# Kernel optimization log

Measured on AMD Instinct MI355X. Metric: run time of the kernel, lower is better.

## Reference

```python
import jax, jax.numpy as jnp
import numpy as np
from jax import lax

BN_EPS = 1e-5


def setup_inputs() -> dict:
    key = jax.random.key(0)
    ks = jax.random.split(key, 8)
    B, C, H, W = 2, 256, 64, 64
    Cr = C // 4
    return {
        "x": jax.random.normal(ks[0], (B, C, H, W), jnp.float32),
        "conv_w": jax.random.normal(ks[1], (Cr, C, 3, 3), jnp.float32) * 0.02,
        "conv_b": jax.random.normal(ks[2], (Cr,), jnp.float32) * 0.02,
        "bn_gamma": jax.random.uniform(ks[3], (Cr,), jnp.float32, 0.5, 1.5),
        "bn_beta": jax.random.normal(ks[4], (Cr,), jnp.float32) * 0.1,
        "bn_mean": jax.random.normal(ks[5], (Cr,), jnp.float32) * 0.1,
        "bn_var": jax.random.uniform(ks[6], (Cr,), jnp.float32, 0.5, 1.5),
        "prelu_w": jnp.full((1,), 0.25, jnp.float32),
    }


def reference(x, conv_w, conv_b, bn_gamma, bn_beta, bn_mean, bn_var, prelu_w):
    B, C, H, W = x.shape
    N = H * W
    # conv_match: 3x3 conv (pad=1) -> BatchNorm (inference) -> PReLU
    y = lax.conv_general_dilated(
        x, conv_w, window_strides=(1, 1), padding="SAME",
        dimension_numbers=("NCHW", "OIHW", "NCHW"))
    y = y + conv_b[None, :, None, None]
    scale = bn_gamma / jnp.sqrt(bn_var + BN_EPS)
    y = (y - bn_mean[None, :, None, None]) * scale[None, :, None, None] + bn_beta[None, :, None, None]
    y = jnp.where(y >= 0, y, prelu_w[0] * y)  # PReLU, single shared slope

    e = y.reshape(B, -1, N)                       # [B, Cr, N]
    sim = jnp.einsum("bdn,bdm->bnm", e, e)        # [B, N, N]
    sim = sim - jnp.max(sim, axis=2, keepdims=True)

    # sparsemax along last dim
    srt = -jnp.sort(-sim, axis=2)                 # descending sort
    cs = jnp.cumsum(srt, axis=2) - 1.0
    ar = jnp.arange(1, N + 1, dtype=sim.dtype)[None, None, :]
    mask = ar * srt > cs
    k = jnp.sum(mask, axis=2, keepdims=True)      # int support size, [B,N,1]
    tau = jnp.take_along_axis(cs, k - 1, axis=2) / k.astype(sim.dtype)
    p = jnp.maximum(sim - tau, 0.0)               # sparsemax probs [B,N,N]

    out = jnp.einsum("bcn,bnm->bcm", x.reshape(B, C, N), p)
    return out.reshape(B, C, H, W) + x
```

## Files before the change

### kernel.cpp

```cpp
#include <hip/hip_runtime.h>
#include <math.h>

#define NPIX 4096
#define CR   64
#define CIN  256
#define HW   64
#define CSPLIT 8

typedef __attribute__((ext_vector_type(8))) short s16x8;
typedef __attribute__((ext_vector_type(4))) float f32x4;

__device__ __forceinline__ unsigned short f2bf(float f) {
  union { float f; unsigned u; } a; a.f = f;
  return (unsigned short)((a.u + 0x7FFF + ((a.u >> 16) & 1)) >> 16);
}
__device__ __forceinline__ float bf2f(unsigned short h) {
  union { unsigned u; float f; } a; a.u = (unsigned)h << 16; return a.f;
}

__global__ __launch_bounds__(256) void k_conv_part(
    const float* __restrict__ x, const float* __restrict__ cw,
    float* __restrict__ pp) {
  const int hg = blockIdx.x;
  const int dg = blockIdx.y;
  const int b  = blockIdx.z >> 3;
  const int cs = blockIdx.z & 7;
  const int h0 = hg * 2, d0 = dg * 32, c0 = cs * 32;
  const int tid = threadIdx.x;
  const int wp = tid & 31;
  const int dq = tid >> 5;
  const int w0 = wp * 2;

  __shared__ float xs[16][4][68];
  __shared__ float wl[16][9][32];

  float acc[2][2][4] = {};

  for (int cc = 0; cc < 32; cc += 16) {
    __syncthreads();
    for (int i = tid; i < 16 * 256; i += 256) {
      int c = i >> 8, r = (i >> 6) & 3, w = i & 63;
      int row = h0 - 1 + r;
      float v = 0.f;
      if (row >= 0 && row < HW)
        v = x[((size_t)(b * CIN + c0 + cc + c) << 12) + row * HW + w];
      xs[c][r][w + 1] = v;
    }
    if (tid < 128) {
      int c = tid >> 3, r = (tid >> 1) & 3, s = tid & 1;
      xs[c][r][s ? 65 : 0] = 0.f;
    }
    for (int i = tid; i < 16 * 9 * 32; i += 256) {
      int c = i / 288, rem = i - c * 288, tap = rem >> 5, d = rem & 31;
      wl[c][tap][d] = cw[(size_t)(d0 + d) * 2304 + (c0 + cc + c) * 9 + tap];
    }
    __syncthreads();

#pragma unroll 2
    for (int c = 0; c < 16; ++c) {
      float xv[4][4];
#pragma unroll
      for (int r = 0; r < 4; ++r) {
        float2 p0 = *(const float2*)&xs[c][r][w0];
        float2 p1 = *(const float2*)&xs[c][r][w0 + 2];
        xv[r][0] = p0.x; xv[r][1] = p0.y; xv[r][2] = p1.x; xv[r][3] = p1.y;
      }
#pragma unroll
      for (int tap = 0; tap < 9; ++tap) {
        const int kh = tap / 3, kw = tap - kh * 3;
        float4 wv = *(const float4*)&wl[c][tap][dq * 4];
        float wf[4] = {wv.x, wv.y, wv.z, wv.w};
#pragma unroll
        for (int hi = 0; hi < 2; ++hi)
#pragma unroll
          for (int wi = 0; wi < 2; ++wi) {
            float xvv = xv[hi + kh][wi + kw];
#pragma unroll
            for (int di = 0; di < 4; ++di)
              acc[hi][wi][di] = fmaf(wf[di], xvv, acc[hi][wi][di]);
          }
      }
    }
  }
#pragma unroll
  for (int di = 0; di < 4; ++di) {
    int d = d0 + dq * 4 + di;
#pragma unroll
    for (int hi = 0; hi < 2; ++hi)
#pragma unroll
      for (int wi = 0; wi < 2; ++wi)
        pp[((size_t)((b * CSPLIT + cs) * 64 + d) << 12) + (h0 + hi) * HW + w0 + wi] =
            acc[hi][wi][di];
  }
}

__global__ __launch_bounds__(256) void k_bn(
    const float* __restrict__ pp, const float* __restrict__ cb,
    const float* __restrict__ gamma, const float* __restrict__ beta,
    const float* __restrict__ mean, const float* __restrict__ var,
    const float* __restrict__ pw, unsigned short* __restrict__ eTh,
    unsigned short* __restrict__ eTl) {
  const int n0 = blockIdx.x * 64;
  const int b  = blockIdx.y;
  const int tid = threadIdx.x;
  __shared__ float et[64][65];

  const float slope = pw[0];
#pragma unroll 4
  for (int dd = 0; dd < 16; ++dd) {
    int d = dd * 4 + (tid >> 6);
    int n = tid & 63;
    float s = 0.f;
#pragma unroll
    for (int cs = 0; cs < CSPLIT; ++cs)
      s += pp[((size_t)((b * CSPLIT + cs) * 64 + d) << 12) + n0 + n];
    float scale = gamma[d] / sqrtf(var[d] + 1e-5f);
    float y = (s + cb[d] - mean[d]) * scale + beta[d];
    y = (y >= 0.f) ? y : slope * y;
    et[d][n] = y;
  }
  __syncthreads();
#pragma unroll 4
  for (int w = 0; w < 16; ++w) {
    int n = w * 4 + (tid >> 6);
    int d = tid & 63;
    float v = et[d][n];
    unsigned short hi = f2bf(v);
    unsigned short lo = f2bf(v - bf2f(hi));
    int nl = n0 + n;
    int g = nl >> 8, i = nl & 255;
    int np = (g << 8) | ((i & 15) << 4) | (i >> 4);
    size_t off = (((size_t)b << 12) + np) * 64 + d;
    eTh[off] = hi;
    eTl[off] = lo;
  }
}

__global__ __launch_bounds__(1024) void k_gsm(
    const unsigned short* __restrict__ eTh, const unsigned short* __restrict__ eTl,
    unsigned short* __restrict__ p, unsigned char* __restrict__ flags) {
  const int n0 = blockIdx.x * 16;
  const int b  = blockIdx.y;
  const int tid = threadIdx.x;
  const int l = tid & 63, wid = tid >> 6;
  const int lc = l & 15, lq = l >> 4;

  __shared__ __align__(16) unsigned short eah[16][72];
  __shared__ __align__(16) unsigned short eal[16][72];
  __shared__ float rs[16][16];
  __shared__ int   rc[16][16];
  __shared__ float stau[16];
  __shared__ int   sprev[16];
  __shared__ int   schg;

  const size_t ebase = ((size_t)b << 12) * 64;

  {
    int d = tid & 63, r = (tid >> 6) & 15;
    int g = n0 >> 8, a = (n0 & 255) >> 4;
    int np = (g << 8) | (r << 4) | a;
    size_t off = ebase + (size_t)np * 64 + d;
    eah[r][d] = eTh[off];
    eal[r][d] = eTl[off];
  }
  if (tid < 16) sprev[tid] = NPIX + 1;
  __syncthreads();

  f32x4 acc[16];
#pragma unroll
  for (int t = 0; t < 16; ++t)
#pragma unroll
    for (int q = 0; q < 4; ++q) acc[t][q] = 0.f;

  const int mbase = wid * 256;
#pragma unroll
  for (int kc = 0; kc < 2; ++kc) {
    s16x8 ah = *(const s16x8*)&eah[lc][kc * 32 + lq * 8];
    s16x8 al = *(const s16x8*)&eal[lc][kc * 32 + lq * 8];
#pragma unroll
    for (int t = 0; t < 16; ++t) {
      size_t off = ebase + (size_t)(mbase + t * 16 + lc) * 64 + kc * 32 + lq * 8;
      s16x8 bh = *(const s16x8*)&eTh[off];
      s16x8 bl = *(const s16x8*)&eTl[off];
      acc[t] = __builtin_amdgcn_mfma_f32_16x16x32_bf16(ah, bh, acc[t], 0, 0, 0);
      acc[t] = __builtin_amdgcn_mfma_f32_16x16x32_bf16(ah, bl, acc[t], 0, 0, 0);
      acc[t] = __builtin_amdgcn_mfma_f32_16x16x32_bf16(al, bh, acc[t], 0, 0, 0);
    }
  }

  {
    float mx[4];
#pragma unroll
    for (int q = 0; q < 4; ++q) {
      float m = acc[0][q];
#pragma unroll
      for (int t = 1; t < 16; ++t) m = fmaxf(m, acc[t][q]);
      mx[q] = m;
    }
#pragma unroll
    for (int o = 1; o <= 8; o <<= 1)
#pragma unroll
      for (int q = 0; q < 4; ++q) mx[q] = fmaxf(mx[q], __shfl_xor(mx[q], o));
    if (lc == 0)
#pragma unroll
      for (int q = 0; q < 4; ++q) rs[wid][lq * 4 + q] = mx[q];
  }
  __syncthreads();
  if (tid < 16) {
    float m = rs[0][tid];
#pragma unroll
    for (int w = 1; w < 16; ++w) m = fmaxf(m, rs[w][tid]);
    stau[tid] = m - 1.0f;
  }

  for (int it = 0; it < 64; ++it) {
    __syncthreads();
    float tl[4];
#pragma unroll
    for (int q = 0; q < 4; ++q) tl[q] = stau[lq * 4 + q];
    if (tid == 0) schg = 0;
    float s[4]; int c[4];
#pragma unroll
    for (int q = 0; q < 4; ++q) { s[q] = 0.f; c[q] = 0; }
#pragma unroll
    for (int t = 0; t < 16; ++t)
#pragma unroll
      for (int q = 0; q < 4; ++q) {
        float v = acc[t][q];
        if (v > tl[q]) { s[q] += v; ++c[q]; }
      }
#pragma unroll
    for (int o = 1; o <= 8; o <<= 1)
#pragma unroll
      for (int q = 0; q < 4; ++q) {
        s[q] += __shfl_xor(s[q], o);
        c[q] += __shfl_xor(c[q], o);
      }
    if (lc == 0)
#pragma unroll
      for (int q = 0; q < 4; ++q) { rs[wid][lq * 4 + q] = s[q]; rc[wid][lq * 4 + q] = c[q]; }
    __syncthreads();
    if (tid < 16) {
      float ss = 0.f; int cc = 0;
#pragma unroll
      for (int w = 0; w < 16; ++w) { ss += rs[w][tid]; cc += rc[w][tid]; }
      stau[tid] = (ss - 1.f) / (float)cc;
      if (cc != sprev[tid]) { sprev[tid] = cc; schg = 1; }
    }
    __syncthreads();
    if (schg == 0) break;
  }

  float tw[4];
#pragma unroll
  for (int q = 0; q < 4; ++q) tw[q] = stau[lq * 4 + q];
  s16x8 oA[4], oB[4];
  int anyL = 0;
#pragma unroll
  for (int q = 0; q < 4; ++q) {
#pragma unroll
    for (int t = 0; t < 8; ++t) {
      float pv = fmaxf(acc[t][q] - tw[q], 0.f);
      anyL |= (pv > 0.f);
      oA[q][t] = (short)f2bf(pv);
    }
#pragma unroll
    for (int t = 0; t < 8; ++t) {
      float pv = fmaxf(acc[t + 8][q] - tw[q], 0.f);
      anyL |= (pv > 0.f);
      oB[q][t] = (short)f2bf(pv);
    }
  }
  unsigned long long bal = __ballot(anyL != 0);
  const unsigned long long M0 = 0x00FF00FF00FF00FFULL;
  bool w0 = (bal & M0) != 0;
  bool w1 = (bal & ~M0) != 0;
  bool mine = (lc < 8) ? w0 : w1;
  if (mine) {
#pragma unroll
    for (int q = 0; q < 4; ++q) {
      unsigned short* pr =
          p + ((size_t)(b * NPIX + n0 + lq * 4 + q) << 12) + mbase + lc * 16;
      *(s16x8*)pr = oA[q];
      *(s16x8*)(pr + 8) = oB[q];
    }
  }
  if (l == 0) {
    int stripe = blockIdx.x;
    if (w0) flags[(b << 13) | ((wid * 2 + 0) << 8) | stripe] = 1;
    if (w1) flags[(b << 13) | ((wid * 2 + 1) << 8) | stripe] = 1;
  }
}

__global__ __launch_bounds__(256) void k_out_mfma(
    const unsigned short* __restrict__ pb, const float* __restrict__ x,
    float* __restrict__ out, const unsigned char* __restrict__ flags) {
  const int m0 = blockIdx.x * 128;
  const int c0 = blockIdx.y * 64;
  const int b  = blockIdx.z;
  const int tid = threadIdx.x;
  const int l = tid & 63, wid = tid >> 6;
  const int wr = wid >> 1, wc = wid & 1;

  __shared__ unsigned short As[64][42];
  __shared__ unsigned short Bs[128][42];
  __shared__ unsigned char fl[256];

  fl[tid] = flags[(b << 13) | (blockIdx.x << 8) | tid];

  f32x4 acc[2][4];
#pragma unroll
  for (int i = 0; i < 2; ++i)
#pragma unroll
    for (int j = 0; j < 4; ++j)
#pragma unroll
      for (int q = 0; q < 4; ++q) acc[i][j][q] = 0.f;

  const int arow = tid >> 2;
  const int akc  = (tid & 3) * 8;
  const float* axsrc = x + ((size_t)(b * CIN + c0 + arow) << 12) + akc;
  const int bm = (tid & 31) * 4;
  const int bk = (tid >> 5) * 4;
  const unsigned short* bsrc = pb + ((size_t)(b * NPIX + bk) << 12) + m0 + bm;
  const int myhalf = bk >> 4;

  __syncthreads();

  for (int k0 = 0; k0 < NPIX; k0 += 32) {
    const int s0 = k0 >> 4;
    const int have0 = fl[s0], have1 = fl[s0 + 1];
    if (!have0 && !have1) continue;
    __syncthreads();
    float4 A0 = *(const float4*)(axsrc + k0);
    float4 A1 = *(const float4*)(axsrc + k0 + 4);
    s16x8 ap;
    ap[0] = (short)f2bf(A0.x); ap[1] = (short)f2bf(A0.y);
    ap[2] = (short)f2bf(A0.z); ap[3] = (short)f2bf(A0.w);
    ap[4] = (short)f2bf(A1.x); ap[5] = (short)f2bf(A1.y);
    ap[6] = (short)f2bf(A1.z); ap[7] = (short)f2bf(A1.w);
    *(s16x8*)&As[arow][akc] = ap;
    if ((myhalf ? have1 : have0)) {
      const unsigned short* bp = bsrc + ((size_t)k0 << 12);
      ushort4 L0 = *(const ushort4*)(bp);
      ushort4 L1 = *(const ushort4*)(bp + 4096);
      ushort4 L2 = *(const ushort4*)(bp + 8192);
      ushort4 L3 = *(const ushort4*)(bp + 12288);
      *(ushort4*)&Bs[bm + 0][bk] = make_ushort4(L0.x, L1.x, L2.x, L3.x);
      *(ushort4*)&Bs[bm + 1][bk] = make_ushort4(L0.y, L1.y, L2.y, L3.y);
      *(ushort4*)&Bs[bm + 2][bk] = make_ushort4(L0.z, L1.z, L2.z, L3.z);
      *(ushort4*)&Bs[bm + 3][bk] = make_ushort4(L0.w, L1.w, L2.w, L3.w);
    } else {
      ushort4 zz = make_ushort4(0, 0, 0, 0);
      *(ushort4*)&Bs[bm + 0][bk] = zz;
      *(ushort4*)&Bs[bm + 1][bk] = zz;
      *(ushort4*)&Bs[bm + 2][bk] = zz;
      *(ushort4*)&Bs[bm + 3][bk] = zz;
    }
    __syncthreads();

    s16x8 a[2], bb[4];
    const int kg = l >> 4;
#pragma unroll
    for (int i = 0; i < 2; ++i) {
      int row = wr * 32 + i * 16 + (l & 15);
      a[i] = *(const s16x8*)&As[row][kg * 8];
    }
#pragma unroll
    for (int j = 0; j < 4; ++j) {
      int n = wc * 64 + j * 16 + (l & 15);
      bb[j] = *(const s16x8*)&Bs[n][kg * 8];
    }
#pragma unroll
    for (int i = 0; i < 2; ++i)
#pragma unroll
      for (int j = 0; j < 4; ++j)
        acc[i][j] = __builtin_amdgcn_mfma_f32_16x16x32_bf16(
            a[i], bb[j], acc[i][j], 0, 0, 0);
  }

#pragma unroll
  for (int i = 0; i < 2; ++i)
#pragma unroll
    for (int j = 0; j < 4; ++j)
#pragma unroll
      for (int q = 0; q < 4; ++q) {
        int c = c0 + wr * 32 + i * 16 + (l >> 4) * 4 + q;
        int m = m0 + wc * 64 + j * 16 + (l & 15);
        size_t off = ((size_t)(b * CIN + c) << 12) + m;
        out[off] = acc[i][j][q] + x[off];
      }
}

extern "C" void kernel_launch(void* const* d_in, const int* in_sizes, int n_in,
                              void* d_out, int out_size, void* d_ws, size_t ws_size,
                              hipStream_t stream) {
  const float* x     = (const float*)d_in[0];
  const float* cw    = (const float*)d_in[1];
  const float* cb    = (const float*)d_in[2];
  const float* gamma = (const float*)d_in[3];
  const float* beta  = (const float*)d_in[4];
  const float* mean  = (const float*)d_in[5];
  const float* var   = (const float*)d_in[6];
  const float* pw    = (const float*)d_in[7];
  float* out = (float*)d_out;

  unsigned short* p_bf = (unsigned short*)d_ws;
  float* pp  = (float*)((char*)d_ws + ((size_t)64 << 20));
  unsigned short* eTh = (unsigned short*)((char*)d_ws + ((size_t)80 << 20));
  unsigned short* eTl = (unsigned short*)((char*)d_ws + ((size_t)81 << 20));
  unsigned char* flags = (unsigned char*)((char*)d_ws + ((size_t)84 << 20));

  hipMemsetAsync(flags, 0, 2 * 32 * 256, stream);
  k_conv_part<<<dim3(32, 2, 16), 256, 0, stream>>>(x, cw, pp);
  k_bn<<<dim3(64, 2), 256, 0, stream>>>(pp, cb, gamma, beta, mean, var, pw,
                                        eTh, eTl);
  k_gsm<<<dim3(NPIX / 16, 2), 1024, 0, stream>>>(eTh, eTl, p_bf, flags);
  k_out_mfma<<<dim3(32, 4, 2), 256, 0, stream>>>(p_bf, x, out, flags);
}
```

Measured before the change: 287.1 us.

## Process 32 query rows per block in similarity-sparsemax kernel to reuse key loads

The fused similarity/sparsemax kernel now handles two 16-row groups per block instead of one. Each loaded key fragment (hi/lo bf16) feeds MFMAs for both groups, which halves global reads of the embedding matrix per output row and halves the grid size. The cost is double the accumulator registers (128 floats per lane) under a 1024-thread launch bound, which risks spills or lower occupancy. Fewer blocks also means less parallelism to hide latency.

After: 371.8 us. 1.29x slower.

```diff
diff --git a/kernel.cpp b/kernel.cpp
--- a/kernel.cpp
+++ b/kernel.cpp
@@ -139,74 +139,95 @@
 __global__ __launch_bounds__(1024) void k_gsm(
     const unsigned short* __restrict__ eTh, const unsigned short* __restrict__ eTl,
     unsigned short* __restrict__ p, unsigned char* __restrict__ flags) {
-  const int n0 = blockIdx.x * 16;
+  const int n0 = blockIdx.x * 32;
   const int b  = blockIdx.y;
   const int tid = threadIdx.x;
   const int l = tid & 63, wid = tid >> 6;
   const int lc = l & 15, lq = l >> 4;
 
-  __shared__ __align__(16) unsigned short eah[16][72];
-  __shared__ __align__(16) unsigned short eal[16][72];
-  __shared__ float rs[16][16];
-  __shared__ int   rc[16][16];
-  __shared__ float stau[16];
-  __shared__ int   sprev[16];
+  __shared__ __align__(16) unsigned short eah[32][72];
+  __shared__ __align__(16) unsigned short eal[32][72];
+  __shared__ float rs[16][32];
+  __shared__ int   rc[16][32];
+  __shared__ float stau[32];
+  __shared__ int   sprev[32];
   __shared__ int   schg;
 
   const size_t ebase = ((size_t)b << 12) * 64;
 
-  {
-    int d = tid & 63, r = (tid >> 6) & 15;
-    int g = n0 >> 8, a = (n0 & 255) >> 4;
-    int np = (g << 8) | (r << 4) | a;
+  for (int idx = tid; idx < 32 * 64; idx += 1024) {
+    int d = idx & 63, r = idx >> 6;
+    int nl = n0 + r;
+    int g = nl >> 8, i = nl & 255;
+    int np = (g << 8) | ((i & 15) << 4) | (i >> 4);
     size_t off = ebase + (size_t)np * 64 + d;
     eah[r][d] = eTh[off];
     eal[r][d] = eTl[off];
   }
-  if (tid < 16) sprev[tid] = NPIX + 1;
+  if (tid < 32) sprev[tid] = NPIX + 1;
   __syncthreads();
 
-  f32x4 acc[16];
-#pragma unroll
-  for (int t = 0; t < 16; ++t)
-#pragma unroll
-    for (int q = 0; q < 4; ++q) acc[t][q] = 0.f;
+  s16x8 Ah[2][2], Al[2][2];
+#pragma unroll
+  for (int g = 0; g < 2; ++g)
+#pragma unroll
+    for (int kc = 0; kc < 2; ++kc) {
+      Ah[g][kc] = *(const s16x8*)&eah[g * 16 + lc][kc * 32 + lq * 8];
+      Al[g][kc] = *(const s16x8*)&eal[g * 16 + lc][kc * 32 + lq * 8];
+    }
+
+  f32x4 acc[2][16];
+#pragma unroll
+  for (int g = 0; g < 2; ++g)
+#pragma unroll
+    for (int t = 0; t < 16; ++t)
+#pragma unroll
+      for (int q = 0; q < 4; ++q) acc[g][t][q] = 0.f;
 
   const int mbase = wid * 256;
-#pragma unroll
-  for (int kc = 0; kc < 2; ++kc) {
-    s16x8 ah = *(const s16x8*)&eah[lc][kc * 32 + lq * 8];
-    s16x8 al = *(const s16x8*)&eal[lc][kc * 32 + lq * 8];
-#pragma unroll
-    for (int t = 0; t < 16; ++t) {
-      size_t off = ebase + (size_t)(mbase + t * 16 + lc) * 64 + kc * 32 + lq * 8;
-      s16x8 bh = *(const s16x8*)&eTh[off];
-      s16x8 bl = *(const s16x8*)&eTl[off];
-      acc[t] = __builtin_amdgcn_mfma_f32_16x16x32_bf16(ah, bh, acc[t], 0, 0, 0);
-      acc[t] = __builtin_amdgcn_mfma_f32_16x16x32_bf16(ah, bl, acc[t], 0, 0, 0);
-      acc[t] = __builtin_amdgcn_mfma_f32_16x16x32_bf16(al, bh, acc[t], 0, 0, 0);
+#pragma unroll 4
+  for (int t = 0; t < 16; ++t) {
+    size_t off = ebase + (size_t)(mbase + t * 16 + lc) * 64 + lq * 8;
+    s16x8 bh0 = *(const s16x8*)&eTh[off];
+    s16x8 bh1 = *(const s16x8*)&eTh[off + 32];
+    s16x8 bl0 = *(const s16x8*)&eTl[off];
+    s16x8 bl1 = *(const s16x8*)&eTl[off + 32];
+#pragma unroll
+    for (int g = 0; g < 2; ++g) {
+      acc[g][t] = __builtin_amdgcn_mfma_f32_16x16x32_bf16(Ah[g][0], bh0, acc[g][t], 0, 0, 0);
+      acc[g][t] = __builtin_amdgcn_mfma_f32_16x16x32_bf16(Ah[g][0], bl0, acc[g][t], 0, 0, 0);
+      acc[g][t] = __builtin_amdgcn_mfma_f32_16x16x32_bf16(Al[g][0], bh0, acc[g][t], 0, 0, 0);
+      acc[g][t] = __builtin_amdgcn_mfma_f32_16x16x32_bf16(Ah[g][1], bh1, acc[g][t], 0, 0, 0);
+      acc[g][t] = __builtin_amdgcn_mfma_f32_16x16x32_bf16(Ah[g][1], bl1, acc[g][t], 0, 0, 0);
+      acc[g][t] = __builtin_amdgcn_mfma_f32_16x16x32_bf16(Al[g][1], bh1, acc[g][t], 0, 0, 0);
     }
   }
 
   {
-    float mx[4];
-#pragma unroll
-    for (int q = 0; q < 4; ++q) {
-      float m = acc[0][q];
-#pragma unroll
-      for (int t = 1; t < 16; ++t) m = fmaxf(m, acc[t][q]);
-      mx[q] = m;
-    }
+    float mx[2][4];
+#pragma unroll
+    for (int g = 0; g < 2; ++g)
+#pragma unroll
+      for (int q = 0; q < 4; ++q) {
+        float m = acc[g][0][q];
+#pragma unroll
+        for (int t = 1; t < 16; ++t) m = fmaxf(m, acc[g][t][q]);
+        mx[g][q] = m;
+      }
 #pragma unroll
     for (int o = 1; o <= 8; o <<= 1)
 #pragma unroll
-      for (int q = 0; q < 4; ++q) mx[q] = fmaxf(mx[q], __shfl_xor(mx[q], o));
+      for (int g = 0; g < 2; ++g)
+#pragma unroll
+        for (int q = 0; q < 4; ++q) mx[g][q] = fmaxf(mx[g][q], __shfl_xor(mx[g][q], o));
     if (lc == 0)
 #pragma unroll
-      for (int q = 0; q < 4; ++q) rs[wid][lq * 4 + q] = mx[q];
+      for (int g = 0; g < 2; ++g)
+#pragma unroll
+        for (int q = 0; q < 4; ++q) rs[wid][g * 16 + lq * 4 + q] = mx[g][q];
   }
   __syncthreads();
-  if (tid < 16) {
+  if (tid < 32) {
     float m = rs[0][tid];
 #pragma unroll
     for (int w = 1; w < 16; ++w) m = fmaxf(m, rs[w][tid]);
@@ -215,32 +236,45 @@
 
   for (int it = 0; it < 64; ++it) {
     __syncthreads();
-    float tl[4];
-#pragma unroll
-    for (int q = 0; q < 4; ++q) tl[q] = stau[lq * 4 + q];
+    float tl[2][4];
+#pragma unroll
+    for (int g = 0; g < 2; ++g)
+#pragma unroll
+      for (int q = 0; q < 4; ++q) tl[g][q] = stau[g * 16 + lq * 4 + q];
     if (tid == 0) schg = 0;
-    float s[4]; int c[4];
-#pragma unroll
-    for (int q = 0; q < 4; ++q) { s[q] = 0.f; c[q] = 0; }
+    float s[2][4]; int c[2][4];
+#pragma unroll
+    for (int g = 0; g < 2; ++g)
+#pragma unroll
+      for (int q = 0; q < 4; ++q) { s[g][q] = 0.f; c[g][q] = 0; }
 #pragma unroll
     for (int t = 0; t < 16; ++t)
 #pragma unroll
-      for (int q = 0; q < 4; ++q) {
-        float v = acc[t][q];
-        if (v > tl[q]) { s[q] += v; ++c[q]; }
-      }
+      for (int g = 0; g < 2; ++g)
+#pragma unroll
+        for (int q = 0; q < 4; ++q) {
+          float v = acc[g][t][q];
+          if (v > tl[g][q]) { s[g][q] += v; ++c[g][q]; }
+        }
 #pragma unroll
     for (int o = 1; o <= 8; o <<= 1)
 #pragma unroll
-      for (int q = 0; q < 4; ++q) {
-        s[q] += __shfl_xor(s[q], o);
-        c[q] += __shfl_xor(c[q], o);
-      }
+      for (int g = 0; g < 2; ++g)
+#pragma unroll
+        for (int q = 0; q < 4; ++q) {
+          s[g][q] += __shfl_xor(s[g][q], o);
+          c[g][q] += __shfl_xor(c[g][q], o);
+        }
     if (lc == 0)
 #pragma unroll
-      for (int q = 0; q < 4; ++q) { rs[wid][lq * 4 + q] = s[q]; rc[wid][lq * 4 + q] = c[q]; }
-    __syncthreads();
-    if (tid < 16) {
+      for (int g = 0; g < 2; ++g)
+#pragma unroll
+        for (int q = 0; q < 4; ++q) {
+          rs[wid][g * 16 + lq * 4 + q] = s[g][q];
+          rc[wid][g * 16 + lq * 4 + q] = c[g][q];
+        }
+    __syncthreads();
+    if (tid < 32) {
       float ss = 0.f; int cc = 0;
 #pragma unroll
       for (int w = 0; w < 16; ++w) { ss += rs[w][tid]; cc += rc[w][tid]; }
@@ -251,44 +285,49 @@
     if (schg == 0) break;
   }
 
-  float tw[4];
-#pragma unroll
-  for (int q = 0; q < 4; ++q) tw[q] = stau[lq * 4 + q];
-  s16x8 oA[4], oB[4];
-  int anyL = 0;
-#pragma unroll
-  for (int q = 0; q < 4; ++q) {
-#pragma unroll
-    for (int t = 0; t < 8; ++t) {
-      float pv = fmaxf(acc[t][q] - tw[q], 0.f);
-      anyL |= (pv > 0.f);
-      oA[q][t] = (short)f2bf(pv);
-    }
-#pragma unroll
-    for (int t = 0; t < 8; ++t) {
-      float pv = fmaxf(acc[t + 8][q] - tw[q], 0.f);
-      anyL |= (pv > 0.f);
-      oB[q][t] = (short)f2bf(pv);
-    }
-  }
-  unsigned long long bal = __ballot(anyL != 0);
+  float tw[2][4];
+#pragma unroll
+  for (int g = 0; g < 2; ++g)
+#pragma unroll
+    for (int q = 0; q < 4; ++q) tw[g][q] = stau[g * 16 + lq * 4 + q];
   const unsigned long long M0 = 0x00FF00FF00FF00FFULL;
-  bool w0 = (bal & M0) != 0;
-  bool w1 = (bal & ~M0) != 0;
-  bool mine = (lc < 8) ? w0 : w1;
-  if (mine) {
+#pragma unroll
+  for (int g = 0; g < 2; ++g) {
+    s16x8 oA[4], oB[4];
+    int anyL = 0;
 #pragma unroll
     for (int q = 0; q < 4; ++q) {
-      unsigned short* pr =
-          p + ((size_t)(b * NPIX + n0 + lq * 4 + q) << 12) + mbase + lc * 16;
-      *(s16x8*)pr = oA[q];
-      *(s16x8*)(pr + 8) = oB[q];
-    }
-  }
-  if (l == 0) {
-    int stripe = blockIdx.x;
-    if (w0) flags[(b << 13) | ((wid * 2 + 0) << 8) | stripe] = 1;
-    if (w1) flags[(b << 13) | ((wid * 2 + 1) << 8) | stripe] = 1;
+#pragma unroll
+      for (int t = 0; t < 8; ++t) {
+        float pv = fmaxf(acc[g][t][q] - tw[g][q], 0.f);
+        anyL |= (pv > 0.f);
+        oA[q][t] = (short)f2bf(pv);
+      }
+#pragma unroll
+      for (int t = 0; t < 8; ++t) {
+        float pv = fmaxf(acc[g][t + 8][q] - tw[g][q], 0.f);
+        anyL |= (pv > 0.f);
+        oB[q][t] = (short)f2bf(pv);
+      }
+    }
+    unsigned long long bal = __ballot(anyL != 0);
+    bool w0 = (bal & M0) != 0;
+    bool w1 = (bal & ~M0) != 0;
+    bool mine = (lc < 8) ? w0 : w1;
+    if (mine) {
+#pragma unroll
+      for (int q = 0; q < 4; ++q) {
+        unsigned short* pr =
+            p + ((size_t)(b * NPIX + n0 + g * 16 + lq * 4 + q) << 12) + mbase + lc * 16;
+        *(s16x8*)pr = oA[q];
+        *(s16x8*)(pr + 8) = oB[q];
+      }
+    }
+    if (l == 0) {
+      int stripe = blockIdx.x * 2 + g;
+      if (w0) flags[(b << 13) | ((wid * 2 + 0) << 8) | stripe] = 1;
+      if (w1) flags[(b << 13) | ((wid * 2 + 1) << 8) | stripe] = 1;
+    }
   }
 }
 
@@ -414,6 +453,6 @@
   k_conv_part<<<dim3(32, 2, 16), 256, 0, stream>>>(x, cw, pp);
   k_bn<<<dim3(64, 2), 256, 0, stream>>>(pp, cb, gamma, beta, mean, var, pw,
                                         eTh, eTl);
-  k_gsm<<<dim3(NPIX / 16, 2), 1024, 0, stream>>>(eTh, eTl, p_bf, flags);
+  k_gsm<<<dim3(NPIX / 32, 2), 1024, 0, stream>>>(eTh, eTl, p_bf, flags);
   k_out_mfma<<<dim3(32, 4, 2), 256, 0, stream>>>(p_bf, x, out, flags);
 }
```

## Rewrite 3x3 conv as bf16 MFMA implicit GEMM with split weights

Applied to the files above, without the earlier changes.

Replaces the scalar FP32 FMA convolution with an implicit-GEMM kernel using 16x16x32 bf16 MFMA. A new pre-kernel repacks the conv weights into hi and lo bf16 pairs laid out in MFMA fragment order. The input tile is staged in shared memory as bf16 with halo padding. This cuts conv compute time but adds an extra launch and reduces input precision to bf16, which can shift values near sparsemax thresholds.

Result: faster. 269.4 us (-6.2%).

```diff
diff --git a/kernel.cpp b/kernel.cpp
--- a/kernel.cpp
+++ b/kernel.cpp
@@ -18,80 +18,98 @@
   union { unsigned u; float f; } a; a.u = (unsigned)h << 16; return a.f;
 }
 
-__global__ __launch_bounds__(256) void k_conv_part(
-    const float* __restrict__ x, const float* __restrict__ cw,
-    float* __restrict__ pp) {
-  const int hg = blockIdx.x;
-  const int dg = blockIdx.y;
-  const int b  = blockIdx.z >> 3;
-  const int cs = blockIdx.z & 7;
-  const int h0 = hg * 2, d0 = dg * 32, c0 = cs * 32;
+__global__ __launch_bounds__(256) void k_wsplit(
+    const float* __restrict__ cw, unsigned short* __restrict__ wpkh,
+    unsigned short* __restrict__ wpkl) {
+  int idx = blockIdx.x * 256 + threadIdx.x;
+  if (idx >= 8 * 9 * 4 * 64) return;
+  int l = idx & 63;
+  int dt = (idx >> 6) & 3;
+  int r2 = idx >> 8;
+  int tap = r2 % 9;
+  int cs = r2 / 9;
+  int lc = l & 15, lq = l >> 4;
+  int d = dt * 16 + lc;
+  s16x8 oh, ol;
+#pragma unroll
+  for (int j = 0; j < 8; ++j) {
+    int c = cs * 32 + lq * 8 + j;
+    float w = cw[(size_t)d * 2304 + c * 9 + tap];
+    unsigned short hi = f2bf(w);
+    oh[j] = (short)hi;
+    ol[j] = (short)f2bf(w - bf2f(hi));
+  }
+  *(s16x8*)&wpkh[(size_t)idx * 8] = oh;
+  *(s16x8*)&wpkl[(size_t)idx * 8] = ol;
+}
+
+__global__ __launch_bounds__(256) void k_conv_mfma(
+    const float* __restrict__ x, const unsigned short* __restrict__ wpkh,
+    const unsigned short* __restrict__ wpkl, float* __restrict__ pp) {
+  const int ng = blockIdx.x;
+  const int cs = blockIdx.y;
+  const int b  = blockIdx.z;
+  const int h0 = ng * 4;
+  const int c0 = cs * 32;
   const int tid = threadIdx.x;
-  const int wp = tid & 31;
-  const int dq = tid >> 5;
-  const int w0 = wp * 2;
-
-  __shared__ float xs[16][4][68];
-  __shared__ float wl[16][9][32];
-
-  float acc[2][2][4] = {};
-
-  for (int cc = 0; cc < 32; cc += 16) {
-    __syncthreads();
-    for (int i = tid; i < 16 * 256; i += 256) {
-      int c = i >> 8, r = (i >> 6) & 3, w = i & 63;
-      int row = h0 - 1 + r;
-      float v = 0.f;
-      if (row >= 0 && row < HW)
-        v = x[((size_t)(b * CIN + c0 + cc + c) << 12) + row * HW + w];
-      xs[c][r][w + 1] = v;
-    }
-    if (tid < 128) {
-      int c = tid >> 3, r = (tid >> 1) & 3, s = tid & 1;
-      xs[c][r][s ? 65 : 0] = 0.f;
-    }
-    for (int i = tid; i < 16 * 9 * 32; i += 256) {
-      int c = i / 288, rem = i - c * 288, tap = rem >> 5, d = rem & 31;
-      wl[c][tap][d] = cw[(size_t)(d0 + d) * 2304 + (c0 + cc + c) * 9 + tap];
-    }
-    __syncthreads();
-
-#pragma unroll 2
-    for (int c = 0; c < 16; ++c) {
-      float xv[4][4];
-#pragma unroll
-      for (int r = 0; r < 4; ++r) {
-        float2 p0 = *(const float2*)&xs[c][r][w0];
-        float2 p1 = *(const float2*)&xs[c][r][w0 + 2];
-        xv[r][0] = p0.x; xv[r][1] = p0.y; xv[r][2] = p1.x; xv[r][3] = p1.y;
+  const int l = tid & 63, wid = tid >> 6;
+  const int lc = l & 15, lq = l >> 4;
+
+  __shared__ __align__(16) unsigned short xs[6][66][40];
+
+  for (int i = tid; i < 6 * 66 * 32; i += 256) {
+    int w = i % 66;
+    int t2 = i / 66;
+    int c = t2 & 31;
+    int r = t2 >> 5;
+    int hg = h0 - 1 + r, wg = w - 1;
+    float v = 0.f;
+    if (hg >= 0 && hg < HW && wg >= 0 && wg < HW)
+      v = x[((size_t)(b * CIN + c0 + c) << 12) + hg * HW + wg];
+    xs[r][w][c] = f2bf(v);
+  }
+  __syncthreads();
+
+  f32x4 acc[4][4];
+#pragma unroll
+  for (int dt = 0; dt < 4; ++dt)
+#pragma unroll
+    for (int nt = 0; nt < 4; ++nt)
+#pragma unroll
+      for (int q = 0; q < 4; ++q) acc[dt][nt][q] = 0.f;
+
+#pragma unroll
+  for (int tap = 0; tap < 9; ++tap) {
+    const int kh = tap / 3, kw = tap - kh * 3;
+    s16x8 Ah[4], Al[4];
+#pragma unroll
+    for (int dt = 0; dt < 4; ++dt) {
+      size_t widx = ((size_t)((cs * 9 + tap) * 4 + dt) * 64 + l) * 8;
+      Ah[dt] = *(const s16x8*)&wpkh[widx];
+      Al[dt] = *(const s16x8*)&wpkl[widx];
+    }
+#pragma unroll
+    for (int nt = 0; nt < 4; ++nt) {
+      s16x8 bf = *(const s16x8*)&xs[wid + kh][nt * 16 + lc + kw][lq * 8];
+#pragma unroll
+      for (int dt = 0; dt < 4; ++dt) {
+        acc[dt][nt] = __builtin_amdgcn_mfma_f32_16x16x32_bf16(Ah[dt], bf, acc[dt][nt], 0, 0, 0);
+        acc[dt][nt] = __builtin_amdgcn_mfma_f32_16x16x32_bf16(Al[dt], bf, acc[dt][nt], 0, 0, 0);
       }
-#pragma unroll
-      for (int tap = 0; tap < 9; ++tap) {
-        const int kh = tap / 3, kw = tap - kh * 3;
-        float4 wv = *(const float4*)&wl[c][tap][dq * 4];
-        float wf[4] = {wv.x, wv.y, wv.z, wv.w};
-#pragma unroll
-        for (int hi = 0; hi < 2; ++hi)
-#pragma unroll
-          for (int wi = 0; wi < 2; ++wi) {
-            float xvv = xv[hi + kh][wi + kw];
-#pragma unroll
-            for (int di = 0; di < 4; ++di)
-              acc[hi][wi][di] = fmaf(wf[di], xvv, acc[hi][wi][di]);
-          }
+    }
+  }
+
+  float* pr = pp + ((size_t)((b * CSPLIT + cs) * 64) << 12);
+#pragma unroll
+  for (int dt = 0; dt < 4; ++dt)
+#pragma unroll
+    for (int nt = 0; nt < 4; ++nt)
+#pragma unroll
+      for (int q = 0; q < 4; ++q) {
+        int d = dt * 16 + lq * 4 + q;
+        int n = ng * 256 + wid * 64 + nt * 16 + lc;
+        pr[((size_t)d << 12) + n] = acc[dt][nt][q];
       }
-    }
-  }
-#pragma unroll
-  for (int di = 0; di < 4; ++di) {
-    int d = d0 + dq * 4 + di;
-#pragma unroll
-    for (int hi = 0; hi < 2; ++hi)
-#pragma unroll
-      for (int wi = 0; wi < 2; ++wi)
-        pp[((size_t)((b * CSPLIT + cs) * 64 + d) << 12) + (h0 + hi) * HW + w0 + wi] =
-            acc[hi][wi][di];
-  }
 }
 
 __global__ __launch_bounds__(256) void k_bn(
@@ -409,9 +427,12 @@
   unsigned short* eTh = (unsigned short*)((char*)d_ws + ((size_t)80 << 20));
   unsigned short* eTl = (unsigned short*)((char*)d_ws + ((size_t)81 << 20));
   unsigned char* flags = (unsigned char*)((char*)d_ws + ((size_t)84 << 20));
+  unsigned short* wpkh = (unsigned short*)((char*)d_ws + ((size_t)85 << 20));
+  unsigned short* wpkl = (unsigned short*)((char*)d_ws + ((size_t)86 << 20));
 
   hipMemsetAsync(flags, 0, 2 * 32 * 256, stream);
-  k_conv_part<<<dim3(32, 2, 16), 256, 0, stream>>>(x, cw, pp);
+  k_wsplit<<<72, 256, 0, stream>>>(cw, wpkh, wpkl);
+  k_conv_mfma<<<dim3(16, 8, 2), 256, 0, stream>>>(x, wpkh, wpkl, pp);
   k_bn<<<dim3(64, 2), 256, 0, stream>>>(pp, cb, gamma, beta, mean, var, pw,
                                         eTh, eTl);
   k_gsm<<<dim3(NPIX / 16, 2), 1024, 0, stream>>>(eTh, eTl, p_bf, flags);
```
